# Kernel optimization log

Measured on AMD Instinct MI355X. Metric: run time of the kernel, lower is better.

Reference implementation:

```python
import jax, jax.numpy as jnp
import numpy as np

# --- constants from the source module ---
VS = 10.0          # voltage scale: state stores v/VS
GS = 100.0         # leak conductance scale (g_l / GS used in _i_l)
TAYLOR_EPS = 0.1   # switch to Taylor expansion near removable singularity
HH_GATE_EPS = 1e-5 # clip gates away from {0,1}
DT = 0.02          # HMM observation interval (ode integrated 0 -> DT)
N_STEPS = 10       # multi_step_euler: ConstantStepSize with dt0 = DT/10
# Huys & Paninski / standard HH channel parameters
G_NA, E_NA = 120.0, 50.0
G_K,  E_K  = 36.0, -77.0
G_L,  E_L  = 30.0, -54.387
C_M = 1.0


def _safe_ratio(v, shift):
    # x / (1 - exp(-x/10)) with first-order Taylor (10 + 0.5*x) near x=0.
    # Source uses lax.cond on jnp.any(|x|<eps); elementwise where is the
    # faithful vectorized form for batched states.
    x = v + shift
    exact = x / (1.0 - jnp.exp(-x / 10.0))
    taylor = 10.0 + 0.5 * x
    return jnp.where(jnp.abs(x) < TAYLOR_EPS, taylor, exact)


def _alpha_m(v): return 0.1 * _safe_ratio(v, 35.0)
def _beta_m(v):  return 4.0 * jnp.exp(-(v + 65.0) / 18.0)
def _alpha_n(v): return 0.01 * _safe_ratio(v, 55.0)
def _beta_n(v):  return 0.125 * jnp.exp(-(v + 65.0) / 80.0)
def _alpha_h(v): return 0.07 * jnp.exp(-(v + 50.0) / 20.0)
def _beta_h(v):  return 1.0 / (jnp.exp(-(v + 35.0) / 10.0) + 1.0)


def _vector_field(state, i_ext):
    # state: [B, 4*C] laid out as [v/VS | logit(n) | logit(m) | logit(h)]
    v_s, ln, lm, lh = jnp.split(state, 4, axis=-1)
    v = VS * v_s  # membrane potential in mV, [B, C]
    n = jnp.clip(jax.nn.sigmoid(ln), HH_GATE_EPS, 1.0 - HH_GATE_EPS)
    m = jnp.clip(jax.nn.sigmoid(lm), HH_GATE_EPS, 1.0 - HH_GATE_EPS)
    h = jnp.clip(jax.nn.sigmoid(lh), HH_GATE_EPS, 1.0 - HH_GATE_EPS)

    i_na = G_NA * m**3 * h * (v - E_NA)
    i_k = G_K * n**4 * (v - E_K)
    i_l = (G_L / GS) * (v - E_L)
    dv_s = (i_ext - i_na - i_k - i_l) / (C_M * VS)

    dn = _alpha_n(v) * (1.0 - n) - _beta_n(v) * n
    dm = _alpha_m(v) * (1.0 - m) - _beta_m(v) * m
    dh = _alpha_h(v) * (1.0 - h) - _beta_h(v) * h
    # chain rule into logit space: d logit(x)/dt = dx/dt / (x (1 - x))
    dln = dn / (n * (1.0 - n))
    dlm = dm / (m * (1.0 - m))
    dlh = dh / (h * (1.0 - h))
    return jnp.concatenate([dv_s, dln, dlm, dlh], axis=-1)


def setup_inputs() -> dict:
    key = jax.random.key(0)
    k1, k2, k3 = jax.random.split(key, 3)
    B, C = 32768, 128
    # v near resting potential (-65 mV -> -6.5 in scaled units), gate logits ~ N(0,1)
    v0 = -6.5 + 0.3 * jax.random.normal(k1, (B, C), dtype=jnp.float32)
    gates = jax.random.normal(k2, (B, 3 * C), dtype=jnp.float32)
    state = jnp.concatenate([v0, gates], axis=-1)  # [B, 4C]
    i_ext = 10.0 * jax.random.uniform(k3, (C,), dtype=jnp.float32)
    return {"state": state, "i_ext": i_ext}


def reference(state, i_ext):
    # multi-step Euler: 10 constant steps of DT/10 from t0=0 to t1=DT
    h = DT / N_STEPS

    def step(s, _):
        return s + h * _vector_field(s, i_ext), None

    out, _ = jax.lax.scan(step, state, None, length=N_STEPS)
    return out
```

## Files before the change

kernel.cpp:

```cpp
#include <hip/hip_runtime.h>
#include <stdint.h>

#define LOG2E    1.4426950408889634f
#define NLN2     -0.6931471805599453f
#define NL720    -0.0020037431123457824f
#define QB       -0.07013100893210239f
#define EM2      0.13533528323661270f
#define BN_C     0.08592215f
#define AH_C     0.03306561f
#define BM_C     0.75550365f
#define HSTEP    0.002f
#define HLOG     -0.0028853900817779268f
#define IE_ADJ   16.3161f

__device__ __forceinline__ float bf2f(uint32_t lo16) {
  union { uint32_t u; float f; } c; c.u = lo16 << 16; return c.f;
}

__device__ __forceinline__ void load4(const void* p, int elem_off, bool is_f32,
                                      float* f) {
  if (is_f32) {
    float4 a = *(const float4*)((const float*)p + elem_off);
    f[0] = a.x; f[1] = a.y; f[2] = a.z; f[3] = a.w;
  } else {
    uint2 u = *(const uint2*)((const unsigned short*)p + elem_off);
    f[0] = bf2f(u.x & 0xffffu); f[1] = bf2f(u.x >> 16);
    f[2] = bf2f(u.y & 0xffffu); f[3] = bf2f(u.y >> 16);
  }
}

__global__ __launch_bounds__(256) void hh_kernel(
    const void* __restrict__ state,
    const void* __restrict__ iext,
    float* __restrict__ out,
    int C, int ngroups , int nthreads) {
  uint32_t wi = ((const uint32_t*)iext)[threadIdx.x & 63];
  bool i_f32 = __ballot((wi & 0x8000u) != 0u) != 0ull;
  uint32_t ws = ((const uint32_t*)state)[threadIdx.x & 31];
  bool s_f32 = __ballot(((ws >> 7) & 0xFFu) != 0x81u) != 0ull;

  int g = blockIdx.x * blockDim.x + threadIdx.x;
  if (g >= nthreads) return;
  int b  = g / ngroups;
  int gc = g - b * ngroups;
  int base = b * 4 * C + gc * 4;

  float v[4], ln[4], lm[4], lh[4], ie[4], iep[4];
  load4(state, base,         s_f32, v);
  load4(state, base + C,     s_f32, ln);
  load4(state, base + 2 * C, s_f32, lm);
  load4(state, base + 3 * C, s_f32, lh);
  load4(iext,  gc * 4,       i_f32, ie);
#pragma unroll
  for (int i = 0; i < 4; ++i) {
    v[i]  *= 10.0f;
    ln[i] *= -LOG2E;
    lm[i] *= -LOG2E;
    lh[i] *= -LOG2E;
    iep[i] = ie[i] - IE_ADJ;
  }

#pragma unroll 1
  for (int s = 0; s < 10; ++s) {
#pragma unroll
    for (int i = 0; i < 4; ++i) {
      float en = __builtin_amdgcn_exp2f(ln[i]);
      float em = __builtin_amdgcn_exp2f(lm[i]);
      float eh = __builtin_amdgcn_exp2f(lh[i]);
      float qq = __builtin_amdgcn_exp2f(__builtin_fmaf(v[i], NL720, QB));

      float q2 = qq * qq, q4 = q2 * q2, q8 = q4 * q4, q9 = q8 * qq;
      float q18 = q9 * q9, q36 = q18 * q18, q40 = q36 * q4, q72 = q36 * q36;
      float e1 = q72;
      float bn = BN_C * q9;
      float ah = AH_C * q36;
      float bm = BM_C * q40;

      float x1 = __builtin_fmaf(0.1f,  v[i], 3.5f);
      float x2 = __builtin_fmaf(0.01f, v[i], 0.55f);
      bool  t1 = fabsf(x1) < 0.01f;
      bool  t2 = fabsf(x2) < 0.001f;

      float d1 = 1.0f + en, d2 = 1.0f + em, d3 = 1.0f + eh;
      float d7 = t1 ? 1.0f : (1.0f - e1);
      float d8 = t2 ? 1.0f : __builtin_fmaf(-EM2, e1, 1.0f);
      float f6 = (1.0f + e1) * eh;

      float p2 = d1 * d2, p3 = p2 * d3, p4 = p3 * en;
      float p5 = p4 * em, p6 = p5 * f6, p7 = p6 * d7, p8 = p7 * d8;
      float r  = __builtin_amdgcn_rcpf(p8);
      float ian_ = r * p7;  r *= d8;
      float iam_ = r * p6;  r *= d7;
      float i9e  = r * p5;  r *= f6;
      float iem  = r * p4;  r *= em;
      float ien  = r * p3;  r *= en;
      float hg   = r * p2;  r *= d3;
      float m    = r * d1;  r *= d2;
      float n    = r;

      float m3h = m * m * m * hg;
      float n4  = n * n; n4 *= n4;
      float ga  = __builtin_fmaf(120.0f, m3h, 0.3f);
      ga = __builtin_fmaf(36.0f, n4, ga);
      float gb  = __builtin_fmaf(6000.0f, m3h, iep[i]);
      gb = __builtin_fmaf(-2772.0f, n4, gb);
      float dv  = __builtin_fmaf(-v[i], ga, gb);

      float am = t1 ? __builtin_fmaf(0.5f, x1, 1.0f) : x1 * iam_;
      float an = t2 ? __builtin_fmaf(0.5f, x2, 0.1f) : x2 * ian_;

      float dln = d1 * __builtin_fmaf(-bn, ien, an);
      float dlm = d2 * __builtin_fmaf(-bm, iem, am);
      float dlh = d3 * (ah - i9e);

      v[i]  = __builtin_fmaf(HSTEP, dv,  v[i]);
      ln[i] = __builtin_fmaf(HLOG,  dln, ln[i]);
      lm[i] = __builtin_fmaf(HLOG,  dlm, lm[i]);
      lh[i] = __builtin_fmaf(HLOG,  dlh, lh[i]);
    }
  }

#pragma unroll
  for (int i = 0; i < 4; ++i) {
    v[i]  *= 0.1f;
    ln[i] *= NLN2;
    lm[i] *= NLN2;
    lh[i] *= NLN2;
  }
  *(float4*)(out + base)         = make_float4(v[0],  v[1],  v[2],  v[3]);
  *(float4*)(out + base + C)     = make_float4(ln[0], ln[1], ln[2], ln[3]);
  *(float4*)(out + base + 2 * C) = make_float4(lm[0], lm[1], lm[2], lm[3]);
  *(float4*)(out + base + 3 * C) = make_float4(lh[0], lh[1], lh[2], lh[3]);
}

extern "C" void kernel_launch(void* const* d_in, const int* in_sizes, int n_in,
                              void* d_out, int out_size, void* d_ws, size_t ws_size,
                              hipStream_t stream) {
  const void* state = d_in[0];
  const void* iext  = d_in[1];
  float* out = (float*)d_out;

  int C = in_sizes[1];
  int cells = in_sizes[0] / 4;
  int nthreads = cells / 4;
  int ngroups = C / 4;
  int block = 256;
  int grid = (nthreads + block - 1) / block;
  hh_kernel<<<grid, block, 0, stream>>>(state, iext, out, C, ngroups, nthreads);
}
```

Measured before the change: 147.8 us.

## Process one cell per thread instead of four with scalar loads

Each thread now integrates a single cell instead of four, so there are four times as many threads. Vectorized float4 loads and stores become scalar coalesced accesses, and a shift/mask index path replaces the division when C is a power of two. The aim is more parallelism and wave occupancy for this compute-bound exp-heavy loop. In exchange it gives up the per-thread instruction-level parallelism from interleaving four independent cells, and uses narrower memory transactions.

```diff
diff --git a/kernel.cpp b/kernel.cpp
--- a/kernel.cpp
+++ b/kernel.cpp
@@ -17,23 +17,16 @@
   union { uint32_t u; float f; } c; c.u = lo16 << 16; return c.f;
 }
 
-__device__ __forceinline__ void load4(const void* p, int elem_off, bool is_f32,
-                                      float* f) {
-  if (is_f32) {
-    float4 a = *(const float4*)((const float*)p + elem_off);
-    f[0] = a.x; f[1] = a.y; f[2] = a.z; f[3] = a.w;
-  } else {
-    uint2 u = *(const uint2*)((const unsigned short*)p + elem_off);
-    f[0] = bf2f(u.x & 0xffffu); f[1] = bf2f(u.x >> 16);
-    f[2] = bf2f(u.y & 0xffffu); f[3] = bf2f(u.y >> 16);
-  }
+__device__ __forceinline__ float load1(const void* p, int elem_off, bool is_f32) {
+  if (is_f32) return ((const float*)p)[elem_off];
+  return bf2f(((const unsigned short*)p)[elem_off]);
 }
 
 __global__ __launch_bounds__(256) void hh_kernel(
     const void* __restrict__ state,
     const void* __restrict__ iext,
     float* __restrict__ out,
-    int C, int ngroups , int nthreads) {
+    int C, int lg , int nthreads) {
   uint32_t wi = ((const uint32_t*)iext)[threadIdx.x & 63];
   bool i_f32 = __ballot((wi & 0x8000u) != 0u) != 0ull;
   uint32_t ws = ((const uint32_t*)state)[threadIdx.x & 31];
@@ -41,96 +34,83 @@
 
   int g = blockIdx.x * blockDim.x + threadIdx.x;
   if (g >= nthreads) return;
-  int b  = g / ngroups;
-  int gc = g - b * ngroups;
-  int base = b * 4 * C + gc * 4;
+  int b, c;
+  if (lg >= 0) {
+    b = g >> lg;
+    c = g & (C - 1);
+  } else {
+    b = g / C;
+    c = g - b * C;
+  }
+  int base = b * 4 * C + c;
 
-  float v[4], ln[4], lm[4], lh[4], ie[4], iep[4];
-  load4(state, base,         s_f32, v);
-  load4(state, base + C,     s_f32, ln);
-  load4(state, base + 2 * C, s_f32, lm);
-  load4(state, base + 3 * C, s_f32, lh);
-  load4(iext,  gc * 4,       i_f32, ie);
-#pragma unroll
-  for (int i = 0; i < 4; ++i) {
-    v[i]  *= 10.0f;
-    ln[i] *= -LOG2E;
-    lm[i] *= -LOG2E;
-    lh[i] *= -LOG2E;
-    iep[i] = ie[i] - IE_ADJ;
-  }
+  float v  = load1(state, base,         s_f32) * 10.0f;
+  float ln = load1(state, base + C,     s_f32) * -LOG2E;
+  float lm = load1(state, base + 2 * C, s_f32) * -LOG2E;
+  float lh = load1(state, base + 3 * C, s_f32) * -LOG2E;
+  float iep = load1(iext, c, i_f32) - IE_ADJ;
 
 #pragma unroll 1
   for (int s = 0; s < 10; ++s) {
-#pragma unroll
-    for (int i = 0; i < 4; ++i) {
-      float en = __builtin_amdgcn_exp2f(ln[i]);
-      float em = __builtin_amdgcn_exp2f(lm[i]);
-      float eh = __builtin_amdgcn_exp2f(lh[i]);
-      float qq = __builtin_amdgcn_exp2f(__builtin_fmaf(v[i], NL720, QB));
+    float en = __builtin_amdgcn_exp2f(ln);
+    float em = __builtin_amdgcn_exp2f(lm);
+    float eh = __builtin_amdgcn_exp2f(lh);
+    float qq = __builtin_amdgcn_exp2f(__builtin_fmaf(v, NL720, QB));
 
-      float q2 = qq * qq, q4 = q2 * q2, q8 = q4 * q4, q9 = q8 * qq;
-      float q18 = q9 * q9, q36 = q18 * q18, q40 = q36 * q4, q72 = q36 * q36;
-      float e1 = q72;
-      float bn = BN_C * q9;
-      float ah = AH_C * q36;
-      float bm = BM_C * q40;
+    float q2 = qq * qq, q4 = q2 * q2, q8 = q4 * q4, q9 = q8 * qq;
+    float q18 = q9 * q9, q36 = q18 * q18, q40 = q36 * q4, q72 = q36 * q36;
+    float e1 = q72;
+    float bn = BN_C * q9;
+    float ah = AH_C * q36;
+    float bm = BM_C * q40;
 
-      float x1 = __builtin_fmaf(0.1f,  v[i], 3.5f);
-      float x2 = __builtin_fmaf(0.01f, v[i], 0.55f);
-      bool  t1 = fabsf(x1) < 0.01f;
-      bool  t2 = fabsf(x2) < 0.001f;
+    float x1 = __builtin_fmaf(0.1f,  v, 3.5f);
+    float x2 = __builtin_fmaf(0.01f, v, 0.55f);
+    bool  t1 = fabsf(x1) < 0.01f;
+    bool  t2 = fabsf(x2) < 0.001f;
 
-      float d1 = 1.0f + en, d2 = 1.0f + em, d3 = 1.0f + eh;
-      float d7 = t1 ? 1.0f : (1.0f - e1);
-      float d8 = t2 ? 1.0f : __builtin_fmaf(-EM2, e1, 1.0f);
-      float f6 = (1.0f + e1) * eh;
+    float d1 = 1.0f + en, d2 = 1.0f + em, d3 = 1.0f + eh;
+    float d7 = t1 ? 1.0f : (1.0f - e1);
+    float d8 = t2 ? 1.0f : __builtin_fmaf(-EM2, e1, 1.0f);
+    float f6 = (1.0f + e1) * eh;
 
-      float p2 = d1 * d2, p3 = p2 * d3, p4 = p3 * en;
-      float p5 = p4 * em, p6 = p5 * f6, p7 = p6 * d7, p8 = p7 * d8;
-      float r  = __builtin_amdgcn_rcpf(p8);
-      float ian_ = r * p7;  r *= d8;
-      float iam_ = r * p6;  r *= d7;
-      float i9e  = r * p5;  r *= f6;
-      float iem  = r * p4;  r *= em;
-      float ien  = r * p3;  r *= en;
-      float hg   = r * p2;  r *= d3;
-      float m    = r * d1;  r *= d2;
-      float n    = r;
+    float p2 = d1 * d2, p3 = p2 * d3, p4 = p3 * en;
+    float p5 = p4 * em, p6 = p5 * f6, p7 = p6 * d7, p8 = p7 * d8;
+    float r  = __builtin_amdgcn_rcpf(p8);
+    float ian_ = r * p7;  r *= d8;
+    float iam_ = r * p6;  r *= d7;
+    float i9e  = r * p5;  r *= f6;
+    float iem  = r * p4;  r *= em;
+    float ien  = r * p3;  r *= en;
+    float hg   = r * p2;  r *= d3;
+    float m    = r * d1;  r *= d2;
+    float n    = r;
 
-      float m3h = m * m * m * hg;
-      float n4  = n * n; n4 *= n4;
-      float ga  = __builtin_fmaf(120.0f, m3h, 0.3f);
-      ga = __builtin_fmaf(36.0f, n4, ga);
-      float gb  = __builtin_fmaf(6000.0f, m3h, iep[i]);
-      gb = __builtin_fmaf(-2772.0f, n4, gb);
-      float dv  = __builtin_fmaf(-v[i], ga, gb);
+    float m3h = m * m * m * hg;
+    float n4  = n * n; n4 *= n4;
+    float ga  = __builtin_fmaf(120.0f, m3h, 0.3f);
+    ga = __builtin_fmaf(36.0f, n4, ga);
+    float gb  = __builtin_fmaf(6000.0f, m3h, iep);
+    gb = __builtin_fmaf(-2772.0f, n4, gb);
+    float dv  = __builtin_fmaf(-v, ga, gb);
 
-      float am = t1 ? __builtin_fmaf(0.5f, x1, 1.0f) : x1 * iam_;
-      float an = t2 ? __builtin_fmaf(0.5f, x2, 0.1f) : x2 * ian_;
+    float am = t1 ? __builtin_fmaf(0.5f, x1, 1.0f) : x1 * iam_;
+    float an = t2 ? __builtin_fmaf(0.5f, x2, 0.1f) : x2 * ian_;
 
-      float dln = d1 * __builtin_fmaf(-bn, ien, an);
-      float dlm = d2 * __builtin_fmaf(-bm, iem, am);
-      float dlh = d3 * (ah - i9e);
+    float dln = d1 * __builtin_fmaf(-bn, ien, an);
+    float dlm = d2 * __builtin_fmaf(-bm, iem, am);
+    float dlh = d3 * (ah - i9e);
 
-      v[i]  = __builtin_fmaf(HSTEP, dv,  v[i]);
-      ln[i] = __builtin_fmaf(HLOG,  dln, ln[i]);
-      lm[i] = __builtin_fmaf(HLOG,  dlm, lm[i]);
-      lh[i] = __builtin_fmaf(HLOG,  dlh, lh[i]);
-    }
+    v  = __builtin_fmaf(HSTEP, dv,  v);
+    ln = __builtin_fmaf(HLOG,  dln, ln);
+    lm = __builtin_fmaf(HLOG,  dlm, lm);
+    lh = __builtin_fmaf(HLOG,  dlh, lh);
   }
 
-#pragma unroll
-  for (int i = 0; i < 4; ++i) {
-    v[i]  *= 0.1f;
-    ln[i] *= NLN2;
-    lm[i] *= NLN2;
-    lh[i] *= NLN2;
-  }
-  *(float4*)(out + base)         = make_float4(v[0],  v[1],  v[2],  v[3]);
-  *(float4*)(out + base + C)     = make_float4(ln[0], ln[1], ln[2], ln[3]);
-  *(float4*)(out + base + 2 * C) = make_float4(lm[0], lm[1], lm[2], lm[3]);
-  *(float4*)(out + base + 3 * C) = make_float4(lh[0], lh[1], lh[2], lh[3]);
+  out[base]         = v  * 0.1f;
+  out[base + C]     = ln * NLN2;
+  out[base + 2 * C] = lm * NLN2;
+  out[base + 3 * C] = lh * NLN2;
 }
 
 extern "C" void kernel_launch(void* const* d_in, const int* in_sizes, int n_in,
@@ -142,9 +122,13 @@
 
   int C = in_sizes[1];
   int cells = in_sizes[0] / 4;
-  int nthreads = cells / 4;
-  int ngroups = C / 4;
+  int nthreads = cells;
+  int lg = -1;
+  if ((C & (C - 1)) == 0) {
+    lg = 0;
+    while ((1 << lg) < C) ++lg;
+  }
   int block = 256;
   int grid = (nthreads + block - 1) / block;
-  hh_kernel<<<grid, block, 0, stream>>>(state, iext, out, C, ngroups, nthreads);
+  hh_kernel<<<grid, block, 0, stream>>>(state, iext, out, C, lg, nthreads);
 }
```

Measured after the change: 177.9 us. +20.4%, slower.
